# Kernel tuning notes

Measured on AMD Instinct MI355X. Metric: run time of the kernel, lower is better.

## Reference

```python
import jax, jax.numpy as jnp
import numpy as np

D_MODEL = 1024
NUM_HEADS = 16
D_K = D_MODEL // NUM_HEADS
B, S = 2, 2048


def setup_inputs() -> dict:
    key = jax.random.key(0)
    ks = jax.random.split(key, 4)
    scale = 1.0 / np.sqrt(D_MODEL)
    x = jax.random.normal(ks[0], (B, S, D_MODEL), dtype=jnp.float32)
    w_qkv = jax.random.normal(ks[1], (D_MODEL, 3 * D_MODEL), dtype=jnp.float32) * scale
    b_qkv = jnp.zeros((3 * D_MODEL,), dtype=jnp.float32)
    w_out = jax.random.normal(ks[2], (D_MODEL, D_MODEL), dtype=jnp.float32) * scale
    b_out = jnp.zeros((D_MODEL,), dtype=jnp.float32)
    # causal mask: 1 where attention is allowed (j <= i), 0 elsewhere
    mask = jnp.tril(jnp.ones((S, S), dtype=jnp.int32))
    return {"x": x, "mask": mask, "w_qkv": w_qkv, "b_qkv": b_qkv,
            "w_out": w_out, "b_out": b_out}


def reference(x, mask, w_qkv, b_qkv, w_out, b_out):
    Bb, Ss, C = x.shape
    qkv = x @ w_qkv + b_qkv                      # [B,S,3C]
    q, k, v = jnp.split(qkv, 3, axis=-1)
    def split_heads(t):
        return t.reshape(Bb, Ss, NUM_HEADS, D_K).transpose(0, 2, 1, 3)  # [B,H,S,Dk]
    q, k, v = split_heads(q), split_heads(k), split_heads(v)
    scores = jnp.einsum('bhqd,bhkd->bhqk', q, k) / jnp.sqrt(jnp.float32(D_K))
    scores = jnp.where(mask == 0, -jnp.inf, scores)
    weights = jax.nn.softmax(scores, axis=-1)
    weights = jnp.nan_to_num(weights, nan=0.0)   # matches torch.nan_to_num
    attn = jnp.einsum('bhqk,bhkd->bhqd', weights, v)
    attn = attn.transpose(0, 2, 1, 3).reshape(Bb, Ss, C)
    return attn @ w_out + b_out
```

## Files before the change

### kernel.cpp

```cpp
#include <hip/hip_runtime.h>
#include <hip/hip_bf16.h>

#define D_MODEL 1024
#define NUM_HEADS 16
#define D_K 64
#define BATCH 2
#define SEQ 2048

typedef __attribute__((ext_vector_type(8))) short bf16x8;
typedef __attribute__((ext_vector_type(4))) float f32x4;

union P16 { int4 i4; ushort u[8]; };
union FU { float f; unsigned int u; };

__device__ __forceinline__ float bf2f(ushort u) {
    union { unsigned int i; float f; } c; c.i = ((unsigned int)u) << 16; return c.f;
}
__device__ __forceinline__ ushort f2bf(float f) {
    union { float f; unsigned int i; } c; c.f = f;
    unsigned int x = c.i;
    return (ushort)((x + 0x7fff + ((x >> 16) & 1)) >> 16);
}

__device__ __forceinline__ bool wave_detect_f32(const ushort* x) {
    ushort u = x[2 * (threadIdx.x & 63)];
    int e = (u >> 7) & 0xFF;
    unsigned long long bl = __ballot(e >= 100 && e <= 141);
    return __popcll(bl) < 32;
}

__global__ __launch_bounds__(256)
void prep_all(const ushort* __restrict__ x, const void* __restrict__ Wq,
              const void* __restrict__ Wo, ushort* __restrict__ xb,
              ushort* __restrict__ WqT, ushort* __restrict__ WoT,
              int* __restrict__ flag)
{
    const bool f32 = wave_detect_f32(x);
    const int bx = blockIdx.x, tx = threadIdx.x;
    if (bx == 0 && tx == 0) flag[0] = f32 ? 1 : 0;

    if (bx >= 1024) {
        if (!f32) return;
        int i = ((bx - 1024) * 256 + tx) * 8;
        const float* f = (const float*)x + i;
        float4 a = *(const float4*)f, b = *(const float4*)(f + 4);
        P16 r;
        r.u[0] = f2bf(a.x); r.u[1] = f2bf(a.y); r.u[2] = f2bf(a.z); r.u[3] = f2bf(a.w);
        r.u[4] = f2bf(b.x); r.u[5] = f2bf(b.y); r.u[6] = f2bf(b.z); r.u[7] = f2bf(b.w);
        *(int4*)(xb + i) = r.i4;
        return;
    }

    __shared__ ushort t[64][72];
    const int nb = bx & 63, kb = bx >> 6;
    const void* W; ushort* WT; int N, n0;
    if (nb < 48) { W = Wq; WT = WqT; N = 3 * D_MODEL; n0 = nb * 64; }
    else         { W = Wo; WT = WoT; N = D_MODEL;     n0 = (nb - 48) * 64; }
    const int k0 = kb * 64, K = D_MODEL;
    #pragma unroll
    for (int p = 0; p < 16; ++p) {
        int r = p * 4 + (tx >> 6), c = tx & 63;
        float v = f32 ? ((const float*)W)[(size_t)(k0 + r) * N + n0 + c]
                      : bf2f(((const ushort*)W)[(size_t)(k0 + r) * N + n0 + c]);
        t[r][c] = f2bf(v);
    }
    __syncthreads();
    #pragma unroll
    for (int p = 0; p < 16; ++p) {
        int nn = p * 4 + (tx >> 6), kk = tx & 63;
        WT[(size_t)(n0 + nn) * K + k0 + kk] = t[kk][nn];
    }
}

template<int MODE>
__global__ __launch_bounds__(256)
void gemm128(const void* __restrict__ Araw, const ushort* __restrict__ Aconv,
             const ushort* __restrict__ WT, const void* __restrict__ bias,
             void* __restrict__ out, int N, int K, const int* __restrict__ flag)
{
    __shared__ ushort As[2][128 * 32];
    __shared__ ushort Bs[2][128 * 32];

    const int f = *flag;
    const ushort* A = (MODE == 1) ? (f ? Aconv : (const ushort*)Araw) : Aconv;

    const int tid = threadIdx.x;
    const int w = tid >> 6, lane = tid & 63;
    const int ln = lane & 15, quad = lane >> 4;
    const int m0 = blockIdx.y * 128, n0 = blockIdx.x * 128;
    const int wm = (w >> 1) * 64, wn = (w & 1) * 64;

    const int s0 = w * 128 + lane, s1 = s0 + 64;
    const int ar0 = s0 >> 2, ak0 = ((s0 & 3) ^ ((ar0 >> 1) & 3)) * 8;
    const int ar1 = s1 >> 2, ak1 = ((s1 & 3) ^ ((ar1 >> 1) & 3)) * 8;
    const size_t aoff0 = (size_t)(m0 + ar0) * K + ak0;
    const size_t aoff1 = (size_t)(m0 + ar1) * K + ak1;
    const size_t boff0 = (size_t)(n0 + ar0) * K + ak0;
    const size_t boff1 = (size_t)(n0 + ar1) * K + ak1;

    const int physc = (quad ^ ((ln >> 1) & 3)) * 8;

    f32x4 acc[4][4] = {};

    const int nk = K >> 5;
    int4 a0 = *(const int4*)(A + aoff0);
    int4 a1 = *(const int4*)(A + aoff1);
    int4 b0 = *(const int4*)(WT + boff0);
    int4 b1 = *(const int4*)(WT + boff1);
    *(int4*)(As[0] + s0 * 8) = a0;
    *(int4*)(As[0] + s1 * 8) = a1;
    *(int4*)(Bs[0] + s0 * 8) = b0;
    *(int4*)(Bs[0] + s1 * 8) = b1;
    a0 = *(const int4*)(A + aoff0 + 32);
    a1 = *(const int4*)(A + aoff1 + 32);
    b0 = *(const int4*)(WT + boff0 + 32);
    b1 = *(const int4*)(WT + boff1 + 32);
    __syncthreads();

    for (int kt = 0; kt < nk; ++kt) {
        const int cur = kt & 1;
        if (kt + 1 < nk) {
            *(int4*)(As[1 - cur] + s0 * 8) = a0;
            *(int4*)(As[1 - cur] + s1 * 8) = a1;
            *(int4*)(Bs[1 - cur] + s0 * 8) = b0;
            *(int4*)(Bs[1 - cur] + s1 * 8) = b1;
        }
        if (kt + 2 < nk) {
            const int kc = (kt + 2) * 32;
            a0 = *(const int4*)(A + aoff0 + kc);
            a1 = *(const int4*)(A + aoff1 + kc);
            b0 = *(const int4*)(WT + boff0 + kc);
            b1 = *(const int4*)(WT + boff1 + kc);
        }

        bf16x8 af[4], bf[4];
        #pragma unroll
        for (int t = 0; t < 4; ++t) {
            af[t] = *(const bf16x8*)(As[cur] + (wm + t * 16 + ln) * 32 + physc);
            bf[t] = *(const bf16x8*)(Bs[cur] + (wn + t * 16 + ln) * 32 + physc);
        }
        #pragma unroll
        for (int mi = 0; mi < 4; ++mi)
            #pragma unroll
            for (int ni = 0; ni < 4; ++ni)
                acc[mi][ni] = __builtin_amdgcn_mfma_f32_16x16x32_bf16(
                    af[mi], bf[ni], acc[mi][ni], 0, 0, 0);
        __syncthreads();
    }

    #pragma unroll
    for (int mi = 0; mi < 4; ++mi) {
        #pragma unroll
        for (int ni = 0; ni < 4; ++ni) {
            int col = n0 + wn + ni * 16 + ln;
            float bb = f ? ((const float*)bias)[col] : bf2f(((const ushort*)bias)[col]);
            #pragma unroll
            for (int r = 0; r < 4; ++r) {
                int row = m0 + wm + mi * 16 + quad * 4 + r;
                float v = acc[mi][ni][r] + bb;
                if (MODE == 0 && f) ((float*)out)[(size_t)row * N + col] = v;
                else                ((ushort*)out)[(size_t)row * N + col] = f2bf(v);
            }
        }
    }
}

template<int MODE>
__global__ __launch_bounds__(256)
void gemm64(const void* __restrict__ Araw, const ushort* __restrict__ Aconv,
            const ushort* __restrict__ WT, const void* __restrict__ bias,
            void* __restrict__ out, int N, int K, const int* __restrict__ flag)
{
    __shared__ ushort As[2][64 * 32];
    __shared__ ushort Bs[2][128 * 32];

    const int f = *flag;
    const ushort* A = (MODE == 1) ? (f ? Aconv : (const ushort*)Araw) : Aconv;

    const int tid = threadIdx.x;
    const int w = tid >> 6, lane = tid & 63;
    const int ln = lane & 15, quad = lane >> 4;
    const int m0 = blockIdx.y * 64, n0 = blockIdx.x * 128;
    const int wn = w * 32;

    const int sa = tid;
    const int arow = sa >> 2, akc = ((sa & 3) ^ ((arow >> 1) & 3)) * 8;
    const size_t aoff = (size_t)(m0 + arow) * K + akc;
    const int sb0 = tid, sb1 = tid + 256;
    const int br0 = sb0 >> 2, bk0 = ((sb0 & 3) ^ ((br0 >> 1) & 3)) * 8;
    const int br1 = sb1 >> 2, bk1 = ((sb1 & 3) ^ ((br1 >> 1) & 3)) * 8;
    const size_t boff0 = (size_t)(n0 + br0) * K + bk0;
    const size_t boff1 = (size_t)(n0 + br1) * K + bk1;

    const int physc = (quad ^ ((ln >> 1) & 3)) * 8;

    f32x4 acc[4][2] = {};

    const int nk = K >> 5;
    int4 a0 = *(const int4*)(A + aoff);
    int4 b0 = *(const int4*)(WT + boff0);
    int4 b1 = *(const int4*)(WT + boff1);
    *(int4*)(As[0] + sa * 8)  = a0;
    *(int4*)(Bs[0] + sb0 * 8) = b0;
    *(int4*)(Bs[0] + sb1 * 8) = b1;
    a0 = *(const int4*)(A + aoff + 32);
    b0 = *(const int4*)(WT + boff0 + 32);
    b1 = *(const int4*)(WT + boff1 + 32);
    __syncthreads();

    for (int kt = 0; kt < nk; ++kt) {
        const int cur = kt & 1;
        if (kt + 1 < nk) {
            *(int4*)(As[1 - cur] + sa * 8)  = a0;
            *(int4*)(Bs[1 - cur] + sb0 * 8) = b0;
            *(int4*)(Bs[1 - cur] + sb1 * 8) = b1;
        }
        if (kt + 2 < nk) {
            const int kc = (kt + 2) * 32;
            a0 = *(const int4*)(A + aoff + kc);
            b0 = *(const int4*)(WT + boff0 + kc);
            b1 = *(const int4*)(WT + boff1 + kc);
        }

        bf16x8 af[4], bf[2];
        #pragma unroll
        for (int t = 0; t < 4; ++t)
            af[t] = *(const bf16x8*)(As[cur] + (t * 16 + ln) * 32 + physc);
        #pragma unroll
        for (int t = 0; t < 2; ++t)
            bf[t] = *(const bf16x8*)(Bs[cur] + (wn + t * 16 + ln) * 32 + physc);
        #pragma unroll
        for (int mi = 0; mi < 4; ++mi)
            #pragma unroll
            for (int ni = 0; ni < 2; ++ni)
                acc[mi][ni] = __builtin_amdgcn_mfma_f32_16x16x32_bf16(
                    af[mi], bf[ni], acc[mi][ni], 0, 0, 0);
        __syncthreads();
    }

    #pragma unroll
    for (int mi = 0; mi < 4; ++mi) {
        #pragma unroll
        for (int ni = 0; ni < 2; ++ni) {
            int col = n0 + wn + ni * 16 + ln;
            float bb = f ? ((const float*)bias)[col] : bf2f(((const ushort*)bias)[col]);
            #pragma unroll
            for (int r = 0; r < 4; ++r) {
                int row = m0 + mi * 16 + quad * 4 + r;
                float v = acc[mi][ni][r] + bb;
                if (MODE == 0 && f) ((float*)out)[(size_t)row * N + col] = v;
                else                ((ushort*)out)[(size_t)row * N + col] = f2bf(v);
            }
        }
    }
}

__global__ __launch_bounds__(256)
void flash_attn7(const ushort* __restrict__ qkv, ushort* __restrict__ attn)
{
    __shared__ ushort Ks[64][72];
    __shared__ ushort Vs[64][72];
    __shared__ ushort QPs[128][72];

    const int tid  = threadIdx.x;
    const int wave = tid >> 6, lane = tid & 63;
    const int ln   = lane & 15, quad = lane >> 4;
    const int pg   = wave >> 1, ww = wave & 1;
    const int bh   = blockIdx.x;
    const int ky   = blockIdx.y;
    const int k    = (ky < 8) ? ky : 23 - ky;
    const int xx   = 2 * k + pg;
    const int b    = bh >> 4, hh = bh & (NUM_HEADS - 1);
    const int W3   = 3 * D_MODEL;
    const size_t hbase = (size_t)b * SEQ * W3 + hh * D_K;

    const int q0A = 32 * (63 - xx), q0B = 32 * xx;
    const int ntA = 32 - k, ntB = k + 1;

    const int qrr = tid >> 1, qcol = (tid & 1) * 32;
    const int ksr = tid >> 2, ksc = (tid & 3) * 16;
    const int vp  = tid & 31, vg = (tid >> 5) * 8;

    {
        const int qpg = qrr >> 6, qmt = (qrr >> 5) & 1, ql = qrr & 31;
        const int qxx = 2 * k + qpg;
        const int grow = qmt ? (32 * qxx + ql) : (32 * (63 - qxx) + ql);
        const ushort* src = qkv + hbase + (size_t)grow * W3 + qcol;
        #pragma unroll
        for (int h = 0; h < 4; ++h) {
            P16 v; v.i4 = *(const int4*)(src + h * 8);
            #pragma unroll
            for (int e = 0; e < 8; ++e) v.u[e] = f2bf(bf2f(v.u[e]) * 0.18033688011f);
            *(int4*)(&QPs[qrr][qcol + h * 8]) = v.i4;
        }
    }
    __syncthreads();
    bf16x8 qf[2][2];
    #pragma unroll
    for (int mt = 0; mt < 2; ++mt)
        #pragma unroll
        for (int s = 0; s < 2; ++s)
            qf[mt][s] = *(const bf16x8*)(&QPs[pg * 64 + mt * 32 + ww * 16 + ln][s * 32 + quad * 8]);

    f32x4 acc_o[2][4] = {};
    f32x4 acc_l[2] = {};

    bf16x8 ones8;
    #pragma unroll
    for (int e = 0; e < 8; ++e) ones8[e] = (short)0x3F80;

    const ushort* Kbase = qkv + hbase + D_MODEL;
    const ushort* Vbase = qkv + hbase + 2 * D_MODEL;

    int4 kreg[2], vreg[2];
    {
        const ushort* ksrc = Kbase + (size_t)ksr * W3 + ksc;
        kreg[0] = *(const int4*)(ksrc);
        kreg[1] = *(const int4*)(ksrc + 8);
        vreg[0] = *(const int4*)(Vbase + (size_t)(2 * vp)     * W3 + vg);
        vreg[1] = *(const int4*)(Vbase + (size_t)(2 * vp + 1) * W3 + vg);
    }

    for (int jt = 0; jt < ntA; ++jt) {
        const int j0 = jt * 64;
        const bool doB = (jt < ntB);
        __syncthreads();

        *(int4*)(&Ks[ksr][ksc])     = kreg[0];
        *(int4*)(&Ks[ksr][ksc + 8]) = kreg[1];
        {
            P16 v0, v1; v0.i4 = vreg[0]; v1.i4 = vreg[1];
            #pragma unroll
            for (int e = 0; e < 8; ++e) {
                unsigned int pack = (unsigned int)v0.u[e] | ((unsigned int)v1.u[e] << 16);
                *(unsigned int*)(&Vs[vg + e][2 * vp]) = pack;
            }
        }
        __syncthreads();

        if (jt + 1 < ntA) {
            const int jn = j0 + 64;
            const ushort* ksrc = Kbase + (size_t)(jn + ksr) * W3 + ksc;
            kreg[0] = *(const int4*)(ksrc);
            kreg[1] = *(const int4*)(ksrc + 8);
            vreg[0] = *(const int4*)(Vbase + (size_t)(jn + 2 * vp)     * W3 + vg);
            vreg[1] = *(const int4*)(Vbase + (size_t)(jn + 2 * vp + 1) * W3 + vg);
        }

        f32x4 sa[2][4];
        #pragma unroll
        for (int t = 0; t < 4; ++t) {
            bf16x8 k0 = *(const bf16x8*)(&Ks[t * 16 + ln][quad * 8]);
            bf16x8 k1 = *(const bf16x8*)(&Ks[t * 16 + ln][32 + quad * 8]);
            {
                f32x4 z = {};
                z = __builtin_amdgcn_mfma_f32_16x16x32_bf16(qf[0][0], k0, z, 0, 0, 0);
                z = __builtin_amdgcn_mfma_f32_16x16x32_bf16(qf[0][1], k1, z, 0, 0, 0);
                sa[0][t] = z;
            }
            if (doB) {
                f32x4 z = {};
                z = __builtin_amdgcn_mfma_f32_16x16x32_bf16(qf[1][0], k0, z, 0, 0, 0);
                z = __builtin_amdgcn_mfma_f32_16x16x32_bf16(qf[1][1], k1, z, 0, 0, 0);
                sa[1][t] = z;
            }
        }

        if (jt == ntA - 1) {
            const int rowb = q0A + ww * 16 + quad * 4;
            #pragma unroll
            for (int t = 0; t < 4; ++t)
                #pragma unroll
                for (int r = 0; r < 4; ++r)
                    if (j0 + t * 16 + ln > rowb + r) sa[0][t][r] = -1e30f;
        }
        if (doB && jt == ntB - 1) {
            const int rowb = q0B + ww * 16 + quad * 4;
            #pragma unroll
            for (int t = 0; t < 4; ++t)
                #pragma unroll
                for (int r = 0; r < 4; ++r)
                    if (j0 + t * 16 + ln > rowb + r) sa[1][t][r] = -1e30f;
        }

        const int lnx = ln ^ ((quad & 1) * 8);
        #pragma unroll
        for (int mt = 0; mt < 2; ++mt) {
            if (mt && !doB) break;
            #pragma unroll
            for (int r = 0; r < 4; ++r) {
                const int prow = pg * 64 + mt * 32 + ww * 16 + quad * 4 + r;
                #pragma unroll
                for (int t = 0; t < 4; ++t) {
                    FU cc; cc.f = exp2f(sa[mt][t][r]);
                    QPs[prow][((t ^ (quad >> 1)) * 16) + lnx] = (ushort)(cc.u >> 16);
                }
            }
        }

        #pragma unroll
        for (int s = 0; s < 2; ++s) {
            const int pcol = s * 32 + ((quad ^ ((ln >> 2) & 3)) * 8);
            bf16x8 pf0 = *(const bf16x8*)(&QPs[pg * 64 + ww * 16 + ln][pcol]);
            bf16x8 pf1;
            if (doB) pf1 = *(const bf16x8*)(&QPs[pg * 64 + 32 + ww * 16 + ln][pcol]);
            #pragma unroll
            for (int t = 0; t < 4; ++t) {
                bf16x8 vf = *(const bf16x8*)(&Vs[t * 16 + ln][s * 32 + quad * 8]);
                acc_o[0][t] = __builtin_amdgcn_mfma_f32_16x16x32_bf16(pf0, vf, acc_o[0][t], 0, 0, 0);
                if (doB)
                    acc_o[1][t] = __builtin_amdgcn_mfma_f32_16x16x32_bf16(pf1, vf, acc_o[1][t], 0, 0, 0);
            }
            acc_l[0] = __builtin_amdgcn_mfma_f32_16x16x32_bf16(pf0, ones8, acc_l[0], 0, 0, 0);
            if (doB)
                acc_l[1] = __builtin_amdgcn_mfma_f32_16x16x32_bf16(pf1, ones8, acc_l[1], 0, 0, 0);
        }
    }

    #pragma unroll
    for (int mt = 0; mt < 2; ++mt) {
        const int q0 = mt ? q0B : q0A;
        #pragma unroll
        for (int r = 0; r < 4; ++r) {
            float inv = 1.0f / acc_l[mt][r];
            int i = q0 + ww * 16 + quad * 4 + r;
            size_t rowoff = ((size_t)(b * SEQ + i)) * D_MODEL + hh * D_K;
            #pragma unroll
            for (int t = 0; t < 4; ++t)
                attn[rowoff + t * 16 + ln] = f2bf(acc_o[mt][t][r] * inv);
        }
    }
}

extern "C" void kernel_launch(void* const* d_in, const int* in_sizes, int n_in,
                              void* d_out, int out_size, void* d_ws, size_t ws_size,
                              hipStream_t stream)
{
    const void* x     = d_in[0];
    const void* w_qkv = d_in[2];
    const void* b_qkv = d_in[3];
    const void* w_out = d_in[4];
    const void* b_out = d_in[5];

    char* ws = (char*)d_ws;
    int*    flag   = (int*)ws;                  size_t off = 256;
    ushort* WqkvT  = (ushort*)(ws + off);       off += (size_t)3 * D_MODEL * D_MODEL * 2;
    ushort* WoutT  = (ushort*)(ws + off);       off += (size_t)D_MODEL * D_MODEL * 2;
    ushort* qkv_ws = (ushort*)(ws + off);       off += (size_t)BATCH * SEQ * 3 * D_MODEL * 2;
    ushort* xb     = (ushort*)(ws + off);
    ushort* attn_ws = xb;

    const int M = BATCH * SEQ;

    prep_all<<<3072, 256, 0, stream>>>((const ushort*)x, w_qkv, w_out,
                                       xb, WqkvT, WoutT, flag);

    gemm128<1><<<dim3(3 * D_MODEL / 128, M / 128), 256, 0, stream>>>(
        x, xb, WqkvT, b_qkv, qkv_ws, 3 * D_MODEL, D_MODEL, flag);

    dim3 ga(BATCH * NUM_HEADS, 16);
    flash_attn7<<<ga, 256, 0, stream>>>(qkv_ws, attn_ws);

    gemm64<0><<<dim3(D_MODEL / 128, M / 64), 256, 0, stream>>>(
        attn_ws, attn_ws, WoutT, b_out, d_out, D_MODEL, D_MODEL, flag);
}
```

Measured before the change: 214.2 us.

## Keep attention probabilities in registers via transposed QK^T MFMA and permuted V

Swaps the MFMA operand order for QK^T so each lane holds scores for one query row across consecutive keys. The exponentiated probabilities can then be packed directly into the bf16 A-operand of the PV MFMA with v_cvt_pk_bf16_f32, with no LDS round-trip. V is stored to shared memory with a permuted key column order so it matches the register layout of P. This removes the per-tile LDS writes and reads of P and the associated bank-conflict swizzling. The risk is that the permutation must exactly match the MFMA fragment layout, or the output is wrong.

```diff
diff --git a/kernel.cpp b/kernel.cpp
--- a/kernel.cpp
+++ b/kernel.cpp
@@ -20,6 +20,11 @@
     union { float f; unsigned int i; } c; c.f = f;
     unsigned int x = c.i;
     return (ushort)((x + 0x7fff + ((x >> 16) & 1)) >> 16);
+}
+__device__ __forceinline__ unsigned int cvt_pk_bf16(float lo, float hi) {
+    unsigned int r;
+    asm("v_cvt_pk_bf16_f32 %0, %1, %2" : "=v"(r) : "v"(lo), "v"(hi));
+    return r;
 }
 
 __device__ __forceinline__ bool wave_detect_f32(const ushort* x) {
@@ -256,7 +261,7 @@
 }
 
 __global__ __launch_bounds__(256)
-void flash_attn7(const ushort* __restrict__ qkv, ushort* __restrict__ attn)
+void flash_attn11(const ushort* __restrict__ qkv, ushort* __restrict__ attn)
 {
     __shared__ ushort Ks[64][72];
     __shared__ ushort Vs[64][72];
@@ -281,6 +286,9 @@
     const int ksr = tid >> 2, ksc = (tid & 3) * 16;
     const int vp  = tid & 31, vg = (tid >> 5) * 8;
 
+    const int vkey = 2 * vp;
+    const int vcol = (vkey & 32) + ((vkey >> 2) & 3) * 8 + ((vkey >> 4) & 1) * 4 + (vkey & 3);
+
     {
         const int qpg = qrr >> 6, qmt = (qrr >> 5) & 1, ql = qrr & 31;
         const int qxx = 2 * k + qpg;
@@ -333,7 +341,7 @@
             #pragma unroll
             for (int e = 0; e < 8; ++e) {
                 unsigned int pack = (unsigned int)v0.u[e] | ((unsigned int)v1.u[e] << 16);
-                *(unsigned int*)(&Vs[vg + e][2 * vp]) = pack;
+                *(unsigned int*)(&Vs[vg + e][vcol]) = pack;
             }
         }
         __syncthreads();
@@ -354,66 +362,65 @@
             bf16x8 k1 = *(const bf16x8*)(&Ks[t * 16 + ln][32 + quad * 8]);
             {
                 f32x4 z = {};
-                z = __builtin_amdgcn_mfma_f32_16x16x32_bf16(qf[0][0], k0, z, 0, 0, 0);
-                z = __builtin_amdgcn_mfma_f32_16x16x32_bf16(qf[0][1], k1, z, 0, 0, 0);
+                z = __builtin_amdgcn_mfma_f32_16x16x32_bf16(k0, qf[0][0], z, 0, 0, 0);
+                z = __builtin_amdgcn_mfma_f32_16x16x32_bf16(k1, qf[0][1], z, 0, 0, 0);
                 sa[0][t] = z;
             }
             if (doB) {
                 f32x4 z = {};
-                z = __builtin_amdgcn_mfma_f32_16x16x32_bf16(qf[1][0], k0, z, 0, 0, 0);
-                z = __builtin_amdgcn_mfma_f32_16x16x32_bf16(qf[1][1], k1, z, 0, 0, 0);
+                z = __builtin_amdgcn_mfma_f32_16x16x32_bf16(k0, qf[1][0], z, 0, 0, 0);
+                z = __builtin_amdgcn_mfma_f32_16x16x32_bf16(k1, qf[1][1], z, 0, 0, 0);
                 sa[1][t] = z;
             }
         }
 
         if (jt == ntA - 1) {
-            const int rowb = q0A + ww * 16 + quad * 4;
+            const int qrow = q0A + ww * 16 + ln;
             #pragma unroll
             for (int t = 0; t < 4; ++t)
                 #pragma unroll
                 for (int r = 0; r < 4; ++r)
-                    if (j0 + t * 16 + ln > rowb + r) sa[0][t][r] = -1e30f;
+                    if (j0 + t * 16 + quad * 4 + r > qrow) sa[0][t][r] = -1e30f;
         }
         if (doB && jt == ntB - 1) {
-            const int rowb = q0B + ww * 16 + quad * 4;
+            const int qrow = q0B + ww * 16 + ln;
             #pragma unroll
             for (int t = 0; t < 4; ++t)
                 #pragma unroll
                 for (int r = 0; r < 4; ++r)
-                    if (j0 + t * 16 + ln > rowb + r) sa[1][t][r] = -1e30f;
-        }
-
-        const int lnx = ln ^ ((quad & 1) * 8);
+                    if (j0 + t * 16 + quad * 4 + r > qrow) sa[1][t][r] = -1e30f;
+        }
+
+        union PB { unsigned int w[4]; bf16x8 v; };
+        PB pa[2][2];
         #pragma unroll
         for (int mt = 0; mt < 2; ++mt) {
             if (mt && !doB) break;
             #pragma unroll
-            for (int r = 0; r < 4; ++r) {
-                const int prow = pg * 64 + mt * 32 + ww * 16 + quad * 4 + r;
+            for (int s = 0; s < 2; ++s) {
                 #pragma unroll
-                for (int t = 0; t < 4; ++t) {
-                    FU cc; cc.f = exp2f(sa[mt][t][r]);
-                    QPs[prow][((t ^ (quad >> 1)) * 16) + lnx] = (ushort)(cc.u >> 16);
+                for (int w = 0; w < 4; ++w) {
+                    const int t = 2 * s + (w >> 1);
+                    const int r0 = (w & 1) * 2;
+                    float lo = exp2f(sa[mt][t][r0]);
+                    float hi = exp2f(sa[mt][t][r0 + 1]);
+                    pa[mt][s].w[w] = cvt_pk_bf16(lo, hi);
                 }
             }
         }
 
         #pragma unroll
         for (int s = 0; s < 2; ++s) {
-            const int pcol = s * 32 + ((quad ^ ((ln >> 2) & 3)) * 8);
-            bf16x8 pf0 = *(const bf16x8*)(&QPs[pg * 64 + ww * 16 + ln][pcol]);
-            bf16x8 pf1;
-            if (doB) pf1 = *(const bf16x8*)(&QPs[pg * 64 + 32 + ww * 16 + ln][pcol]);
             #pragma unroll
             for (int t = 0; t < 4; ++t) {
                 bf16x8 vf = *(const bf16x8*)(&Vs[t * 16 + ln][s * 32 + quad * 8]);
-                acc_o[0][t] = __builtin_amdgcn_mfma_f32_16x16x32_bf16(pf0, vf, acc_o[0][t], 0, 0, 0);
+                acc_o[0][t] = __builtin_amdgcn_mfma_f32_16x16x32_bf16(pa[0][s].v, vf, acc_o[0][t], 0, 0, 0);
                 if (doB)
-                    acc_o[1][t] = __builtin_amdgcn_mfma_f32_16x16x32_bf16(pf1, vf, acc_o[1][t], 0, 0, 0);
-            }
-            acc_l[0] = __builtin_amdgcn_mfma_f32_16x16x32_bf16(pf0, ones8, acc_l[0], 0, 0, 0);
+                    acc_o[1][t] = __builtin_amdgcn_mfma_f32_16x16x32_bf16(pa[1][s].v, vf, acc_o[1][t], 0, 0, 0);
+            }
+            acc_l[0] = __builtin_amdgcn_mfma_f32_16x16x32_bf16(pa[0][s].v, ones8, acc_l[0], 0, 0, 0);
             if (doB)
-                acc_l[1] = __builtin_amdgcn_mfma_f32_16x16x32_bf16(pf1, ones8, acc_l[1], 0, 0, 0);
+                acc_l[1] = __builtin_amdgcn_mfma_f32_16x16x32_bf16(pa[1][s].v, ones8, acc_l[1], 0, 0, 0);
         }
     }
 
@@ -459,7 +466,7 @@
         x, xb, WqkvT, b_qkv, qkv_ws, 3 * D_MODEL, D_MODEL, flag);
 
     dim3 ga(BATCH * NUM_HEADS, 16);
-    flash_attn7<<<ga, 256, 0, stream>>>(qkv_ws, attn_ws);
+    flash_attn11<<<ga, 256, 0, stream>>>(qkv_ws, attn_ws);
 
     gemm64<0><<<dim3(D_MODEL / 128, M / 64), 256, 0, stream>>>(
         attn_ws, attn_ws, WoutT, b_out, d_out, D_MODEL, D_MODEL, flag);
```

Measured after the change: 212.8 us. About the same (-0.6%).
